# Performance work log

Measured on AMD Instinct MI355X. Metric: run time of the kernel, lower is better.

The kernel has to match this reference:

```python
import jax, jax.numpy as jnp
import numpy as np

N_NODES, N_EDGES, B, K, D = 200000, 500000, 8192, 32, 128
E_DIM, E_EMB, N_CLASS = 128, 128, 60


def setup_inputs() -> dict:
    key = jax.random.key(0)
    ks = jax.random.split(key, 16)
    s = lambda k, shape, scale=0.05: jax.random.normal(k, shape, dtype=jnp.float32) * scale
    return {
        'memory_emb': s(ks[0], (N_NODES, D), 1.0),
        'edge_feat': s(ks[1], (N_EDGES, E_DIM), 1.0),
        'W_q': s(ks[2], (D, D)),
        'W_k': s(ks[3], (D, D)),
        'a': s(ks[4], (2 * D,)),
        'We_w': s(ks[5], (E_DIM, E_EMB)),
        'We_b': s(ks[6], (E_EMB,)),
        'Wuc': s(ks[7], (D + 2 * D + E_EMB, D)),
        'Wc1': s(ks[8], (D, 128)),
        'Wc2': s(ks[9], (128, N_CLASS)),
        'src_idxs': jax.random.randint(ks[10], (B,), 0, N_NODES),
        'dst_idxs': jax.random.randint(ks[11], (B,), 0, N_NODES),
        'edge_idxs': jax.random.randint(ks[12], (B,), 0, N_EDGES),
        'src_neighbors': jax.random.randint(ks[13], (B, K), 0, N_NODES),
        'dst_neighbors': jax.random.randint(ks[14], (B, K), 0, N_NODES),
    }


def reference(memory_emb, edge_feat, W_q, W_k, a, We_w, We_b, Wuc, Wc1, Wc2,
              src_idxs, dst_idxs, edge_idxs, src_neighbors, dst_neighbors):
    def attend(idxs, nbrs):
        self_emb = memory_emb[idxs]                      # [B, D] gather
        nb = memory_emb[nbrs]                            # [B, K, D] gather
        q = self_emb @ W_q                               # [B, D]
        k = jnp.einsum('bkd,de->bke', nb, W_k)           # [B, K, D]
        # GAT-style score: leaky_relu(a . [q || k])
        sq = q @ a[:D]                                   # [B]
        sk = jnp.einsum('bkd,d->bk', k, a[D:])           # [B, K]
        score = jax.nn.leaky_relu(sq[:, None] + sk, 0.2)
        attn = jax.nn.softmax(score, axis=-1)            # [B, K]
        agg = jnp.einsum('bk,bkd->bd', attn, k)          # [B, D]
        return self_emb, agg

    src_e, src_h = attend(src_idxs, src_neighbors)
    dst_e, dst_h = attend(dst_idxs, dst_neighbors)
    e = edge_feat[edge_idxs] @ We_w + We_b               # edge embedding [B, E_EMB]
    msg_src = jax.nn.relu(jnp.concatenate([src_e, src_h, dst_h, e], -1) @ Wuc)
    msg_dst = jax.nn.relu(jnp.concatenate([dst_e, dst_h, src_h, e], -1) @ Wuc)
    logits_src = jax.nn.relu(msg_src @ Wc1) @ Wc2
    logits_dst = jax.nn.relu(msg_dst @ Wc1) @ Wc2
    return jnp.stack([logits_src, logits_dst])           # [2, B, N_CLASS]
```

## Files before the change

kernel.cpp:

```cpp
#include <hip/hip_runtime.h>

#define D 128
#define KNBR 32
#define BATCH 8192
#define NCLASS 60

__global__ __launch_bounds__(256) void k_prep(
    const float* __restrict__ Wq, const float* __restrict__ Wk,
    const float* __restrict__ a, const float* __restrict__ Wew,
    const float* __restrict__ Web, const float* __restrict__ Wuc,
    float* __restrict__ wqa, float* __restrict__ wka,
    float* __restrict__ be, float* __restrict__ Wcomb2)
{
    __shared__ float sB[128][129];
    int blk = blockIdx.x, tid = threadIdx.x;
    if (blk == 0) {
        for (int t = tid; t < 128 * 128; t += 256) sB[t >> 7][t & 127] = Wq[t];
        __syncthreads();
        if (tid < 128) {
            float s = 0.f;
            for (int j = 0; j < D; ++j) s += sB[tid][j] * a[j];
            wqa[tid] = s;
        }
        __syncthreads();
        for (int t = tid; t < 128 * 128; t += 256) sB[t >> 7][t & 127] = Wk[t];
        __syncthreads();
        if (tid < 128) {
            float s = 0.f;
            for (int j = 0; j < D; ++j) s += sB[tid][j] * a[D + j];
            wka[tid] = s;
        }
    } else if (blk == 1) {
        if (tid < 128) {
            float acc = 0.f;
            for (int j = 0; j < D; ++j) acc += Web[j] * Wuc[(size_t)(384 + j) * D + tid];
            be[tid] = acc;
        }
    } else {
        int g  = (blk - 2) >> 4;
        int rb = ((blk - 2) & 15) * 8;
        const float* A = (g == 2) ? Wew : Wk;
        const float* B = Wuc + (size_t)(128 + g * 128) * D;
        for (int t = tid; t < 128 * 128; t += 256) sB[t >> 7][t & 127] = B[t];
        __syncthreads();
        int j = tid & 127, half = tid >> 7;
        float acc[4] = {0.f, 0.f, 0.f, 0.f};
        int r0 = rb + half * 4;
        for (int t = 0; t < 128; ++t) {
            float bv = sB[t][j];
            #pragma unroll
            for (int m = 0; m < 4; ++m)
                acc[m] = fmaf(A[(size_t)(r0 + m) * D + t], bv, acc[m]);
        }
        #pragma unroll
        for (int m = 0; m < 4; ++m)
            Wcomb2[(size_t)(g * 128 + r0 + m) * D + j] = acc[m];
    }
}

__global__ __launch_bounds__(256) void k_attend(
    const float* __restrict__ mem,
    const float* __restrict__ wqa, const float* __restrict__ wka,
    const int* __restrict__ src_idxs, const int* __restrict__ dst_idxs,
    const int* __restrict__ src_nb, const int* __restrict__ dst_nb,
    float* __restrict__ nbsumbuf)
{
    int b = blockIdx.x, side = blockIdx.y, tid = threadIdx.x;
    const int* idxs = side ? dst_idxs : src_idxs;
    const int* nbrs = side ? dst_nb  : src_nb;

    __shared__ int   s_idx[KNBR];
    __shared__ float s_nb[KNBR][D];
    __shared__ float s_sk[KNBR];
    __shared__ float s_attn[KNBR];
    __shared__ float s_sq;
    __shared__ float s_part[2][D];

    if (tid < KNBR) s_idx[tid] = nbrs[b * KNBR + tid];
    if (tid < 32) {
        int node = idxs[b];
        float4 self4 = ((const float4*)(mem + (size_t)node * D))[tid];
        float4 wq4   = ((const float4*)wqa)[tid];
        float p = self4.x * wq4.x + self4.y * wq4.y + self4.z * wq4.z + self4.w * wq4.w;
        #pragma unroll
        for (int m = 1; m <= 16; m <<= 1) p += __shfl_xor(p, m, 32);
        if (tid == 0) s_sq = p;
    }
    __syncthreads();

    int c4 = tid & 31;
    int rbase = tid >> 5;
    float4 wk4 = ((const float4*)wka)[c4];
    #pragma unroll
    for (int p = 0; p < 4; ++p) {
        int r = rbase + 8 * p;
        float4 v = ((const float4*)(mem + (size_t)s_idx[r] * D))[c4];
        *(float4*)&s_nb[r][c4 * 4] = v;
        float pr = v.x * wk4.x + v.y * wk4.y + v.z * wk4.z + v.w * wk4.w;
        #pragma unroll
        for (int m = 1; m <= 16; m <<= 1) pr += __shfl_xor(pr, m, 32);
        if (c4 == 0) s_sk[r] = pr;
    }
    __syncthreads();

    if (tid < 32) {
        float x = s_sq + s_sk[tid];
        x = (x >= 0.f) ? x : 0.2f * x;
        float mx = x;
        #pragma unroll
        for (int m = 1; m <= 16; m <<= 1) mx = fmaxf(mx, __shfl_xor(mx, m, 32));
        float e = __expf(x - mx);
        float sum = e;
        #pragma unroll
        for (int m = 1; m <= 16; m <<= 1) sum += __shfl_xor(sum, m, 32);
        s_attn[tid] = e / sum;
    }
    __syncthreads();

    int col = tid & 127, half = tid >> 7;
    float acc = 0.f;
    int k0 = half * 16;
    #pragma unroll
    for (int k = 0; k < 16; ++k) acc = fmaf(s_attn[k0 + k], s_nb[k0 + k][col], acc);
    s_part[half][col] = acc;
    __syncthreads();
    if (tid < 128)
        nbsumbuf[((size_t)side * BATCH + b) * D + tid] = s_part[0][tid] + s_part[1][tid];
}

__global__ __launch_bounds__(256) void k_msg(
    const float* __restrict__ mem, const float* __restrict__ edge_feat,
    const float* __restrict__ Wuc, const float* __restrict__ Wcomb2,
    const float* __restrict__ be,
    const int* __restrict__ src_idxs, const int* __restrict__ dst_idxs,
    const int* __restrict__ edge_idxs,
    const float* __restrict__ nbsumbuf, float* __restrict__ msgbuf)
{
    int side = blockIdx.y;
    int b0 = blockIdx.x * 64;
    int tid = threadIdx.x;

    __shared__ float Ast[32][68];
    __shared__ float Ws[32][128];
    __shared__ int s_bidx[64], s_eidx[64];

    if (tid < 64) {
        s_bidx[tid] = (side ? dst_idxs : src_idxs)[b0 + tid];
        s_eidx[tid] = edge_idxs[b0 + tid];
    }
    __syncthreads();

    int tr = tid >> 4, tc = tid & 15;
    int lc = tid & 31, lr = tid >> 5;
    int wc = tid & 127, wk2 = tid >> 7;
    float acc[4][8];
    #pragma unroll
    for (int i = 0; i < 4; ++i)
        #pragma unroll
        for (int j = 0; j < 8; ++j) acc[i][j] = 0.f;

    for (int kt = 0; kt < 16; ++kt) {
        int seg = kt >> 2, off = (kt & 3) * 32;
        if (seg == 0) {
            #pragma unroll
            for (int p = 0; p < 8; ++p) {
                int r = lr + 8 * p;
                Ast[lc][r] = mem[(size_t)s_bidx[r] * D + off + lc];
            }
        } else if (seg == 1) {
            #pragma unroll
            for (int p = 0; p < 8; ++p) {
                int r = lr + 8 * p;
                Ast[lc][r] = nbsumbuf[((size_t)side * BATCH + b0 + r) * D + off + lc];
            }
        } else if (seg == 2) {
            #pragma unroll
            for (int p = 0; p < 8; ++p) {
                int r = lr + 8 * p;
                Ast[lc][r] = nbsumbuf[((size_t)(1 - side) * BATCH + b0 + r) * D + off + lc];
            }
        } else {
            #pragma unroll
            for (int p = 0; p < 8; ++p) {
                int r = lr + 8 * p;
                Ast[lc][r] = edge_feat[(size_t)s_eidx[r] * D + off + lc];
            }
        }
        int krow0 = kt * 32;
        #pragma unroll
        for (int p = 0; p < 16; ++p) {
            int kk = wk2 + 2 * p;
            int gr = krow0 + kk;
            Ws[kk][wc] = (gr < 128) ? Wuc[(size_t)gr * D + wc]
                                    : Wcomb2[(size_t)(gr - 128) * D + wc];
        }
        __syncthreads();
        #pragma unroll 4
        for (int kk = 0; kk < 32; ++kk) {
            float4 a4 = *(const float4*)&Ast[kk][tr * 4];
            float4 w0 = *(const float4*)&Ws[kk][tc * 4];
            float4 w1 = *(const float4*)&Ws[kk][64 + tc * 4];
            float ar[4] = {a4.x, a4.y, a4.z, a4.w};
            float wr[8] = {w0.x, w0.y, w0.z, w0.w, w1.x, w1.y, w1.z, w1.w};
            #pragma unroll
            for (int i = 0; i < 4; ++i)
                #pragma unroll
                for (int j = 0; j < 8; ++j)
                    acc[i][j] = fmaf(ar[i], wr[j], acc[i][j]);
        }
        __syncthreads();
    }

    float4 bv0 = *(const float4*)&be[tc * 4];
    float4 bv1 = *(const float4*)&be[64 + tc * 4];
    #pragma unroll
    for (int i = 0; i < 4; ++i) {
        size_t row = (size_t)side * BATCH + b0 + tr * 4 + i;
        float4 o0 = make_float4(fmaxf(acc[i][0] + bv0.x, 0.f), fmaxf(acc[i][1] + bv0.y, 0.f),
                                fmaxf(acc[i][2] + bv0.z, 0.f), fmaxf(acc[i][3] + bv0.w, 0.f));
        float4 o1 = make_float4(fmaxf(acc[i][4] + bv1.x, 0.f), fmaxf(acc[i][5] + bv1.y, 0.f),
                                fmaxf(acc[i][6] + bv1.z, 0.f), fmaxf(acc[i][7] + bv1.w, 0.f));
        *(float4*)&msgbuf[row * D + tc * 4] = o0;
        *(float4*)&msgbuf[row * D + 64 + tc * 4] = o1;
    }
}

__global__ __launch_bounds__(256) void k_cls(
    const float* __restrict__ msgbuf, const float* __restrict__ Wc1,
    const float* __restrict__ Wc2, float* __restrict__ out)
{
    int side = blockIdx.y;
    int b0 = blockIdx.x * 32;
    int tid = threadIdx.x;

    __shared__ float Ast[32][36];
    __shared__ float Ws[32][128];
    __shared__ float HsT[128][36];
    __shared__ float Wc2s[128][64];

    for (int t = tid; t < 128 * 60; t += 256) {
        int kk = t / 60, c = t - kk * 60;
        Wc2s[kk][c] = Wc2[t];
    }

    int tr = tid >> 4, tc = tid & 15;
    int lc = tid & 31, lr = tid >> 5;
    int wc = tid & 127, wk2 = tid >> 7;
    float acc[2][8];
    #pragma unroll
    for (int i = 0; i < 2; ++i)
        #pragma unroll
        for (int j = 0; j < 8; ++j) acc[i][j] = 0.f;

    for (int kt = 0; kt < 4; ++kt) {
        int off = kt * 32;
        #pragma unroll
        for (int p = 0; p < 4; ++p) {
            int r = lr + 8 * p;
            Ast[lc][r] = msgbuf[((size_t)side * BATCH + b0 + r) * D + off + lc];
        }
        #pragma unroll
        for (int p = 0; p < 16; ++p) {
            int kk = wk2 + 2 * p;
            Ws[kk][wc] = Wc1[(size_t)(off + kk) * D + wc];
        }
        __syncthreads();
        #pragma unroll 4
        for (int kk = 0; kk < 32; ++kk) {
            float2 a2 = *(const float2*)&Ast[kk][tr * 2];
            float4 w0 = *(const float4*)&Ws[kk][tc * 4];
            float4 w1 = *(const float4*)&Ws[kk][64 + tc * 4];
            float ar[2] = {a2.x, a2.y};
            float wr[8] = {w0.x, w0.y, w0.z, w0.w, w1.x, w1.y, w1.z, w1.w};
            #pragma unroll
            for (int i = 0; i < 2; ++i)
                #pragma unroll
                for (int j = 0; j < 8; ++j)
                    acc[i][j] = fmaf(ar[i], wr[j], acc[i][j]);
        }
        __syncthreads();
    }

    #pragma unroll
    for (int i = 0; i < 2; ++i) {
        int r = tr * 2 + i;
        #pragma unroll
        for (int j = 0; j < 4; ++j) {
            HsT[tc * 4 + j][r]      = fmaxf(acc[i][j], 0.f);
            HsT[64 + tc * 4 + j][r] = fmaxf(acc[i][j + 4], 0.f);
        }
    }
    __syncthreads();

    int r0 = (tid >> 4) * 2;
    int cg = tid & 15;
    int c0 = cg * 4;
    float acc2[2][4];
    #pragma unroll
    for (int i = 0; i < 2; ++i)
        #pragma unroll
        for (int j = 0; j < 4; ++j) acc2[i][j] = 0.f;
    for (int kk = 0; kk < 128; ++kk) {
        float2 h2 = *(const float2*)&HsT[kk][r0];
        float4 w4 = *(const float4*)&Wc2s[kk][c0];
        float wr[4] = {w4.x, w4.y, w4.z, w4.w};
        #pragma unroll
        for (int j = 0; j < 4; ++j) {
            acc2[0][j] = fmaf(h2.x, wr[j], acc2[0][j]);
            acc2[1][j] = fmaf(h2.y, wr[j], acc2[1][j]);
        }
    }
    if (cg < 15) {
        #pragma unroll
        for (int i = 0; i < 2; ++i) {
            size_t row = (size_t)side * BATCH + b0 + r0 + i;
            *(float4*)&out[row * NCLASS + c0] =
                make_float4(acc2[i][0], acc2[i][1], acc2[i][2], acc2[i][3]);
        }
    }
}

extern "C" void kernel_launch(void* const* d_in, const int* in_sizes, int n_in,
                              void* d_out, int out_size, void* d_ws, size_t ws_size,
                              hipStream_t stream) {
    const float* mem       = (const float*)d_in[0];
    const float* edge_feat = (const float*)d_in[1];
    const float* Wq        = (const float*)d_in[2];
    const float* Wk        = (const float*)d_in[3];
    const float* a         = (const float*)d_in[4];
    const float* Wew       = (const float*)d_in[5];
    const float* Web       = (const float*)d_in[6];
    const float* Wuc       = (const float*)d_in[7];
    const float* Wc1       = (const float*)d_in[8];
    const float* Wc2       = (const float*)d_in[9];
    const int* src_idxs    = (const int*)d_in[10];
    const int* dst_idxs    = (const int*)d_in[11];
    const int* edge_idxs   = (const int*)d_in[12];
    const int* src_nb      = (const int*)d_in[13];
    const int* dst_nb      = (const int*)d_in[14];
    float* out = (float*)d_out;

    float* ws = (float*)d_ws;
    float* Wcomb2 = ws;
    float* be     = ws + 49152;
    float* wqa    = ws + 49280;
    float* wka    = ws + 49408;
    float* nbsum  = ws + 49536;
    float* msgbuf = nbsum + 2097152;

    k_prep<<<50, 256, 0, stream>>>(Wq, Wk, a, Wew, Web, Wuc, wqa, wka, be, Wcomb2);
    k_attend<<<dim3(BATCH, 2), 256, 0, stream>>>(mem, wqa, wka,
                                                 src_idxs, dst_idxs, src_nb, dst_nb,
                                                 nbsum);
    k_msg<<<dim3(BATCH / 64, 2), 256, 0, stream>>>(mem, edge_feat, Wuc, Wcomb2, be,
                                                   src_idxs, dst_idxs, edge_idxs,
                                                   nbsum, msgbuf);
    k_cls<<<dim3(BATCH / 32, 2), 256, 0, stream>>>(msgbuf, Wc1, Wc2, out);
}
```

Before: 541.8 us.

## Fuse attention, message and classifier kernels into one per-batch-tile kernel

Replaces the three kernels (attend, message GEMM, classifier) with one kernel that handles 16 batch rows for both sides per block. Attention runs warp-per-row and gathers the neighbor rows twice (once for scores, once for the weighted sum) rather than staging them in shared memory. Intermediate nbsum and message buffers stay in shared memory, which removes their global round trips and the extra launches. In exchange, each block reloads the full Wuc, Wc1 and Wc2 weights for only 32 rows, and neighbor gathers are issued twice.

```diff
diff --git a/kernel.cpp b/kernel.cpp
--- a/kernel.cpp
+++ b/kernel.cpp
@@ -4,6 +4,8 @@
 #define KNBR 32
 #define BATCH 8192
 #define NCLASS 60
+#define NB 16
+#define NP 32
 
 __global__ __launch_bounds__(256) void k_prep(
     const float* __restrict__ Wq, const float* __restrict__ Wk,
@@ -58,53 +60,59 @@
     }
 }
 
-__global__ __launch_bounds__(256) void k_attend(
-    const float* __restrict__ mem,
+__global__ __launch_bounds__(256, 2) void k_fused(
+    const float* __restrict__ mem, const float* __restrict__ edge_feat,
+    const float* __restrict__ Wuc, const float* __restrict__ Wcomb2,
+    const float* __restrict__ be,
     const float* __restrict__ wqa, const float* __restrict__ wka,
+    const float* __restrict__ Wc1, const float* __restrict__ Wc2,
     const int* __restrict__ src_idxs, const int* __restrict__ dst_idxs,
+    const int* __restrict__ edge_idxs,
     const int* __restrict__ src_nb, const int* __restrict__ dst_nb,
-    float* __restrict__ nbsumbuf)
+    float* __restrict__ out)
 {
-    int b = blockIdx.x, side = blockIdx.y, tid = threadIdx.x;
-    const int* idxs = side ? dst_idxs : src_idxs;
-    const int* nbrs = side ? dst_nb  : src_nb;
-
-    __shared__ int   s_idx[KNBR];
-    __shared__ float s_nb[KNBR][D];
-    __shared__ float s_sk[KNBR];
-    __shared__ float s_attn[KNBR];
-    __shared__ float s_sq;
-    __shared__ float s_part[2][D];
-
-    if (tid < KNBR) s_idx[tid] = nbrs[b * KNBR + tid];
-    if (tid < 32) {
-        int node = idxs[b];
-        float4 self4 = ((const float4*)(mem + (size_t)node * D))[tid];
-        float4 wq4   = ((const float4*)wqa)[tid];
-        float p = self4.x * wq4.x + self4.y * wq4.y + self4.z * wq4.z + self4.w * wq4.w;
-        #pragma unroll
-        for (int m = 1; m <= 16; m <<= 1) p += __shfl_xor(p, m, 32);
-        if (tid == 0) s_sq = p;
-    }
-    __syncthreads();
-
-    int c4 = tid & 31;
-    int rbase = tid >> 5;
-    float4 wk4 = ((const float4*)wka)[c4];
-    #pragma unroll
-    for (int p = 0; p < 4; ++p) {
-        int r = rbase + 8 * p;
-        float4 v = ((const float4*)(mem + (size_t)s_idx[r] * D))[c4];
-        *(float4*)&s_nb[r][c4 * 4] = v;
-        float pr = v.x * wk4.x + v.y * wk4.y + v.z * wk4.z + v.w * wk4.w;
-        #pragma unroll
-        for (int m = 1; m <= 16; m <<= 1) pr += __shfl_xor(pr, m, 32);
-        if (c4 == 0) s_sk[r] = pr;
-    }
-    __syncthreads();
-
-    if (tid < 32) {
-        float x = s_sq + s_sk[tid];
+    __shared__ __align__(16) float s_self[NP * 132];
+    __shared__ __align__(16) float s_nbsum[NP * 132];
+    __shared__ __align__(16) float Ast[32 * 33];
+    __shared__ __align__(16) float Ws[32 * 128];
+    __shared__ __align__(16) float msgT[128 * 35];
+    __shared__ int s_eidx[NB];
+
+    int tid = threadIdx.x;
+    int b0 = blockIdx.x * NB;
+    int lane = tid & 31;
+    int grp  = tid >> 5;
+
+    if (tid < NB) s_eidx[tid] = edge_idxs[b0 + tid];
+
+    float4 wq4 = ((const float4*)wqa)[lane];
+    float4 wk4 = ((const float4*)wka)[lane];
+
+    for (int it = 0; it < 4; ++it) {
+        int p = it * 8 + grp;
+        int side = p >> 4;
+        int bb = b0 + (p & 15);
+        int self_idx = (side ? dst_idxs : src_idxs)[bb];
+        int nb_idx = (side ? dst_nb : src_nb)[(size_t)bb * KNBR + lane];
+
+        float4 sv = ((const float4*)(mem + (size_t)self_idx * D))[lane];
+        *(float4*)&s_self[p * 132 + lane * 4] = sv;
+        float sp = sv.x * wq4.x + sv.y * wq4.y + sv.z * wq4.z + sv.w * wq4.w;
+        #pragma unroll
+        for (int m = 1; m <= 16; m <<= 1) sp += __shfl_xor(sp, m, 32);
+        float sq = sp;
+
+        float myscore = 0.f;
+        #pragma unroll 4
+        for (int k = 0; k < KNBR; ++k) {
+            int ik = __shfl(nb_idx, k, 32);
+            float4 v = ((const float4*)(mem + (size_t)ik * D))[lane];
+            float pr = v.x * wk4.x + v.y * wk4.y + v.z * wk4.z + v.w * wk4.w;
+            #pragma unroll
+            for (int m = 1; m <= 16; m <<= 1) pr += __shfl_xor(pr, m, 32);
+            if (k == lane) myscore = pr;
+        }
+        float x = sq + myscore;
         x = (x >= 0.f) ? x : 0.2f * x;
         float mx = x;
         #pragma unroll
@@ -113,209 +121,161 @@
         float sum = e;
         #pragma unroll
         for (int m = 1; m <= 16; m <<= 1) sum += __shfl_xor(sum, m, 32);
-        s_attn[tid] = e / sum;
-    }
-    __syncthreads();
-
-    int col = tid & 127, half = tid >> 7;
-    float acc = 0.f;
-    int k0 = half * 16;
-    #pragma unroll
-    for (int k = 0; k < 16; ++k) acc = fmaf(s_attn[k0 + k], s_nb[k0 + k][col], acc);
-    s_part[half][col] = acc;
-    __syncthreads();
-    if (tid < 128)
-        nbsumbuf[((size_t)side * BATCH + b) * D + tid] = s_part[0][tid] + s_part[1][tid];
-}
-
-__global__ __launch_bounds__(256) void k_msg(
-    const float* __restrict__ mem, const float* __restrict__ edge_feat,
-    const float* __restrict__ Wuc, const float* __restrict__ Wcomb2,
-    const float* __restrict__ be,
-    const int* __restrict__ src_idxs, const int* __restrict__ dst_idxs,
-    const int* __restrict__ edge_idxs,
-    const float* __restrict__ nbsumbuf, float* __restrict__ msgbuf)
-{
-    int side = blockIdx.y;
-    int b0 = blockIdx.x * 64;
-    int tid = threadIdx.x;
-
-    __shared__ float Ast[32][68];
-    __shared__ float Ws[32][128];
-    __shared__ int s_bidx[64], s_eidx[64];
-
-    if (tid < 64) {
-        s_bidx[tid] = (side ? dst_idxs : src_idxs)[b0 + tid];
-        s_eidx[tid] = edge_idxs[b0 + tid];
+        float attn = e / sum;
+
+        float4 acc = make_float4(0.f, 0.f, 0.f, 0.f);
+        #pragma unroll 4
+        for (int k = 0; k < KNBR; ++k) {
+            int ik = __shfl(nb_idx, k, 32);
+            float ak = __shfl(attn, k, 32);
+            float4 v = ((const float4*)(mem + (size_t)ik * D))[lane];
+            acc.x = fmaf(ak, v.x, acc.x);
+            acc.y = fmaf(ak, v.y, acc.y);
+            acc.z = fmaf(ak, v.z, acc.z);
+            acc.w = fmaf(ak, v.w, acc.w);
+        }
+        *(float4*)&s_nbsum[p * 132 + lane * 4] = acc;
     }
     __syncthreads();
 
     int tr = tid >> 4, tc = tid & 15;
     int lc = tid & 31, lr = tid >> 5;
     int wc = tid & 127, wk2 = tid >> 7;
-    float acc[4][8];
+    float accB[2][8];
     #pragma unroll
-    for (int i = 0; i < 4; ++i)
-        #pragma unroll
-        for (int j = 0; j < 8; ++j) acc[i][j] = 0.f;
+    for (int i = 0; i < 2; ++i)
+        #pragma unroll
+        for (int j = 0; j < 8; ++j) accB[i][j] = 0.f;
 
     for (int kt = 0; kt < 16; ++kt) {
         int seg = kt >> 2, off = (kt & 3) * 32;
-        if (seg == 0) {
-            #pragma unroll
-            for (int p = 0; p < 8; ++p) {
-                int r = lr + 8 * p;
-                Ast[lc][r] = mem[(size_t)s_bidx[r] * D + off + lc];
+        #pragma unroll
+        for (int q = 0; q < 4; ++q) {
+            int r = lr + 8 * q;
+            float v;
+            if (seg == 0)      v = s_self[r * 132 + off + lc];
+            else if (seg == 1) v = s_nbsum[r * 132 + off + lc];
+            else if (seg == 2) v = s_nbsum[(r ^ 16) * 132 + off + lc];
+            else               v = edge_feat[(size_t)s_eidx[r & 15] * D + off + lc];
+            Ast[lc * 33 + r] = v;
+        }
+        int krow0 = kt * 32;
+        #pragma unroll
+        for (int pp = 0; pp < 16; ++pp) {
+            int kk = wk2 + 2 * pp;
+            int gr = krow0 + kk;
+            Ws[kk * 128 + wc] = (gr < 128) ? Wuc[(size_t)gr * D + wc]
+                                           : Wcomb2[(size_t)(gr - 128) * D + wc];
+        }
+        __syncthreads();
+        #pragma unroll 8
+        for (int kk = 0; kk < 32; ++kk) {
+            float a0 = Ast[kk * 33 + tr * 2];
+            float a1 = Ast[kk * 33 + tr * 2 + 1];
+            float4 w0 = *(const float4*)&Ws[kk * 128 + tc * 4];
+            float4 w1 = *(const float4*)&Ws[kk * 128 + 64 + tc * 4];
+            float wr[8] = {w0.x, w0.y, w0.z, w0.w, w1.x, w1.y, w1.z, w1.w};
+            #pragma unroll
+            for (int j = 0; j < 8; ++j) {
+                accB[0][j] = fmaf(a0, wr[j], accB[0][j]);
+                accB[1][j] = fmaf(a1, wr[j], accB[1][j]);
             }
-        } else if (seg == 1) {
-            #pragma unroll
-            for (int p = 0; p < 8; ++p) {
-                int r = lr + 8 * p;
-                Ast[lc][r] = nbsumbuf[((size_t)side * BATCH + b0 + r) * D + off + lc];
+        }
+        __syncthreads();
+    }
+    {
+        float4 bv0 = *(const float4*)&be[tc * 4];
+        float4 bv1 = *(const float4*)&be[64 + tc * 4];
+        float b8[8] = {bv0.x, bv0.y, bv0.z, bv0.w, bv1.x, bv1.y, bv1.z, bv1.w};
+        #pragma unroll
+        for (int i = 0; i < 2; ++i) {
+            int r = tr * 2 + i;
+            #pragma unroll
+            for (int j = 0; j < 4; ++j) {
+                msgT[(tc * 4 + j) * 35 + r]        = fmaxf(accB[i][j] + b8[j], 0.f);
+                msgT[(64 + tc * 4 + j) * 35 + r]   = fmaxf(accB[i][j + 4] + b8[j + 4], 0.f);
             }
-        } else if (seg == 2) {
-            #pragma unroll
-            for (int p = 0; p < 8; ++p) {
-                int r = lr + 8 * p;
-                Ast[lc][r] = nbsumbuf[((size_t)(1 - side) * BATCH + b0 + r) * D + off + lc];
-            }
-        } else {
-            #pragma unroll
-            for (int p = 0; p < 8; ++p) {
-                int r = lr + 8 * p;
-                Ast[lc][r] = edge_feat[(size_t)s_eidx[r] * D + off + lc];
-            }
-        }
-        int krow0 = kt * 32;
-        #pragma unroll
-        for (int p = 0; p < 16; ++p) {
-            int kk = wk2 + 2 * p;
-            int gr = krow0 + kk;
-            Ws[kk][wc] = (gr < 128) ? Wuc[(size_t)gr * D + wc]
-                                    : Wcomb2[(size_t)(gr - 128) * D + wc];
-        }
-        __syncthreads();
-        #pragma unroll 4
-        for (int kk = 0; kk < 32; ++kk) {
-            float4 a4 = *(const float4*)&Ast[kk][tr * 4];
-            float4 w0 = *(const float4*)&Ws[kk][tc * 4];
-            float4 w1 = *(const float4*)&Ws[kk][64 + tc * 4];
-            float ar[4] = {a4.x, a4.y, a4.z, a4.w};
-            float wr[8] = {w0.x, w0.y, w0.z, w0.w, w1.x, w1.y, w1.z, w1.w};
-            #pragma unroll
-            for (int i = 0; i < 4; ++i)
-                #pragma unroll
-                for (int j = 0; j < 8; ++j)
-                    acc[i][j] = fmaf(ar[i], wr[j], acc[i][j]);
-        }
-        __syncthreads();
-    }
-
-    float4 bv0 = *(const float4*)&be[tc * 4];
-    float4 bv1 = *(const float4*)&be[64 + tc * 4];
-    #pragma unroll
-    for (int i = 0; i < 4; ++i) {
-        size_t row = (size_t)side * BATCH + b0 + tr * 4 + i;
-        float4 o0 = make_float4(fmaxf(acc[i][0] + bv0.x, 0.f), fmaxf(acc[i][1] + bv0.y, 0.f),
-                                fmaxf(acc[i][2] + bv0.z, 0.f), fmaxf(acc[i][3] + bv0.w, 0.f));
-        float4 o1 = make_float4(fmaxf(acc[i][4] + bv1.x, 0.f), fmaxf(acc[i][5] + bv1.y, 0.f),
-                                fmaxf(acc[i][6] + bv1.z, 0.f), fmaxf(acc[i][7] + bv1.w, 0.f));
-        *(float4*)&msgbuf[row * D + tc * 4] = o0;
-        *(float4*)&msgbuf[row * D + 64 + tc * 4] = o1;
-    }
-}
-
-__global__ __launch_bounds__(256) void k_cls(
-    const float* __restrict__ msgbuf, const float* __restrict__ Wc1,
-    const float* __restrict__ Wc2, float* __restrict__ out)
-{
-    int side = blockIdx.y;
-    int b0 = blockIdx.x * 32;
-    int tid = threadIdx.x;
-
-    __shared__ float Ast[32][36];
-    __shared__ float Ws[32][128];
-    __shared__ float HsT[128][36];
-    __shared__ float Wc2s[128][64];
-
-    for (int t = tid; t < 128 * 60; t += 256) {
-        int kk = t / 60, c = t - kk * 60;
-        Wc2s[kk][c] = Wc2[t];
-    }
-
-    int tr = tid >> 4, tc = tid & 15;
-    int lc = tid & 31, lr = tid >> 5;
-    int wc = tid & 127, wk2 = tid >> 7;
-    float acc[2][8];
+        }
+    }
+    __syncthreads();
+
+    float accC[2][8];
     #pragma unroll
     for (int i = 0; i < 2; ++i)
         #pragma unroll
-        for (int j = 0; j < 8; ++j) acc[i][j] = 0.f;
+        for (int j = 0; j < 8; ++j) accC[i][j] = 0.f;
 
     for (int kt = 0; kt < 4; ++kt) {
         int off = kt * 32;
         #pragma unroll
-        for (int p = 0; p < 4; ++p) {
-            int r = lr + 8 * p;
-            Ast[lc][r] = msgbuf[((size_t)side * BATCH + b0 + r) * D + off + lc];
-        }
-        #pragma unroll
-        for (int p = 0; p < 16; ++p) {
-            int kk = wk2 + 2 * p;
-            Ws[kk][wc] = Wc1[(size_t)(off + kk) * D + wc];
-        }
-        __syncthreads();
-        #pragma unroll 4
+        for (int pp = 0; pp < 16; ++pp) {
+            int kk = wk2 + 2 * pp;
+            Ws[kk * 128 + wc] = Wc1[(size_t)(off + kk) * D + wc];
+        }
+        __syncthreads();
+        #pragma unroll 8
         for (int kk = 0; kk < 32; ++kk) {
-            float2 a2 = *(const float2*)&Ast[kk][tr * 2];
-            float4 w0 = *(const float4*)&Ws[kk][tc * 4];
-            float4 w1 = *(const float4*)&Ws[kk][64 + tc * 4];
-            float ar[2] = {a2.x, a2.y};
+            float a0 = msgT[(off + kk) * 35 + tr * 2];
+            float a1 = msgT[(off + kk) * 35 + tr * 2 + 1];
+            float4 w0 = *(const float4*)&Ws[kk * 128 + tc * 4];
+            float4 w1 = *(const float4*)&Ws[kk * 128 + 64 + tc * 4];
             float wr[8] = {w0.x, w0.y, w0.z, w0.w, w1.x, w1.y, w1.z, w1.w};
             #pragma unroll
-            for (int i = 0; i < 2; ++i)
-                #pragma unroll
-                for (int j = 0; j < 8; ++j)
-                    acc[i][j] = fmaf(ar[i], wr[j], acc[i][j]);
-        }
-        __syncthreads();
-    }
-
+            for (int j = 0; j < 8; ++j) {
+                accC[0][j] = fmaf(a0, wr[j], accC[0][j]);
+                accC[1][j] = fmaf(a1, wr[j], accC[1][j]);
+            }
+        }
+        __syncthreads();
+    }
     #pragma unroll
     for (int i = 0; i < 2; ++i) {
         int r = tr * 2 + i;
         #pragma unroll
         for (int j = 0; j < 4; ++j) {
-            HsT[tc * 4 + j][r]      = fmaxf(acc[i][j], 0.f);
-            HsT[64 + tc * 4 + j][r] = fmaxf(acc[i][j + 4], 0.f);
+            msgT[(tc * 4 + j) * 35 + r]      = fmaxf(accC[i][j], 0.f);
+            msgT[(64 + tc * 4 + j) * 35 + r] = fmaxf(accC[i][j + 4], 0.f);
         }
     }
     __syncthreads();
 
-    int r0 = (tid >> 4) * 2;
-    int cg = tid & 15;
-    int c0 = cg * 4;
-    float acc2[2][4];
+    int r2 = tid & 31;
+    int cs = tid >> 5;
+    float acc2[8];
     #pragma unroll
-    for (int i = 0; i < 2; ++i)
-        #pragma unroll
-        for (int j = 0; j < 4; ++j) acc2[i][j] = 0.f;
-    for (int kk = 0; kk < 128; ++kk) {
-        float2 h2 = *(const float2*)&HsT[kk][r0];
-        float4 w4 = *(const float4*)&Wc2s[kk][c0];
-        float wr[4] = {w4.x, w4.y, w4.z, w4.w};
-        #pragma unroll
-        for (int j = 0; j < 4; ++j) {
-            acc2[0][j] = fmaf(h2.x, wr[j], acc2[0][j]);
-            acc2[1][j] = fmaf(h2.y, wr[j], acc2[1][j]);
-        }
-    }
-    if (cg < 15) {
-        #pragma unroll
-        for (int i = 0; i < 2; ++i) {
-            size_t row = (size_t)side * BATCH + b0 + r0 + i;
-            *(float4*)&out[row * NCLASS + c0] =
-                make_float4(acc2[i][0], acc2[i][1], acc2[i][2], acc2[i][3]);
+    for (int j = 0; j < 8; ++j) acc2[j] = 0.f;
+
+    for (int kt = 0; kt < 4; ++kt) {
+        int off = kt * 32;
+        for (int t = tid; t < 32 * 64; t += 256) {
+            int kk = t >> 6, c = t & 63;
+            Ws[t] = (c < NCLASS) ? Wc2[(size_t)(off + kk) * NCLASS + c] : 0.f;
+        }
+        __syncthreads();
+        #pragma unroll 4
+        for (int kk = 0; kk < 32; ++kk) {
+            float h = msgT[(off + kk) * 35 + r2];
+            float4 w0 = *(const float4*)&Ws[kk * 64 + cs * 8];
+            float4 w1 = *(const float4*)&Ws[kk * 64 + cs * 8 + 4];
+            acc2[0] = fmaf(h, w0.x, acc2[0]);
+            acc2[1] = fmaf(h, w0.y, acc2[1]);
+            acc2[2] = fmaf(h, w0.z, acc2[2]);
+            acc2[3] = fmaf(h, w0.w, acc2[3]);
+            acc2[4] = fmaf(h, w1.x, acc2[4]);
+            acc2[5] = fmaf(h, w1.y, acc2[5]);
+            acc2[6] = fmaf(h, w1.z, acc2[6]);
+            acc2[7] = fmaf(h, w1.w, acc2[7]);
+        }
+        __syncthreads();
+    }
+    {
+        int side = r2 >> 4;
+        int bb = b0 + (r2 & 15);
+        size_t orow = ((size_t)side * BATCH + bb) * NCLASS;
+        #pragma unroll
+        for (int j = 0; j < 8; ++j) {
+            int c = cs * 8 + j;
+            if (c < NCLASS) out[orow + c] = acc2[j];
         }
     }
 }
@@ -345,15 +305,10 @@
     float* be     = ws + 49152;
     float* wqa    = ws + 49280;
     float* wka    = ws + 49408;
-    float* nbsum  = ws + 49536;
-    float* msgbuf = nbsum + 2097152;
 
     k_prep<<<50, 256, 0, stream>>>(Wq, Wk, a, Wew, Web, Wuc, wqa, wka, be, Wcomb2);
-    k_attend<<<dim3(BATCH, 2), 256, 0, stream>>>(mem, wqa, wka,
-                                                 src_idxs, dst_idxs, src_nb, dst_nb,
-                                                 nbsum);
-    k_msg<<<dim3(BATCH / 64, 2), 256, 0, stream>>>(mem, edge_feat, Wuc, Wcomb2, be,
-                                                   src_idxs, dst_idxs, edge_idxs,
-                                                   nbsum, msgbuf);
-    k_cls<<<dim3(BATCH / 32, 2), 256, 0, stream>>>(msgbuf, Wc1, Wc2, out);
+    k_fused<<<BATCH / NB, 256, 0, stream>>>(mem, edge_feat, Wuc, Wcomb2, be,
+                                            wqa, wka, Wc1, Wc2,
+                                            src_idxs, dst_idxs, edge_idxs,
+                                            src_nb, dst_nb, out);
 }
```

After: 550.5 us. No clear change (+1.6%).
